# Kernel tuning notes

Measured on AMD Instinct MI355X. Metric: run time of the kernel, lower is better.

The kernel has to match this reference:

```python
import jax, jax.numpy as jnp
import numpy as np

C = 256
C8 = C // 8


def setup_inputs() -> dict:
    key = jax.random.key(0)
    ks = jax.random.split(key, 9)
    B, H, W = 4, 64, 64
    inp = jax.random.normal(ks[0], (B, C, H, W), dtype=jnp.float32)
    original = jax.random.normal(ks[1], (B, C, H, W), dtype=jnp.float32)
    s = 1.0 / np.sqrt(C)
    wq = jax.random.normal(ks[2], (C8, C), dtype=jnp.float32) * s
    bq = jax.random.normal(ks[3], (C8,), dtype=jnp.float32) * 0.01
    wk = jax.random.normal(ks[4], (C8, C), dtype=jnp.float32) * s
    bk = jax.random.normal(ks[5], (C8,), dtype=jnp.float32) * 0.01
    wv = jax.random.normal(ks[6], (C, C), dtype=jnp.float32) * s
    bv = jax.random.normal(ks[7], (C,), dtype=jnp.float32) * 0.01
    # torch inits gamma to 0; use a nonzero value so the attention branch contributes
    gamma = jnp.asarray([0.5], dtype=jnp.float32)
    return {"input": inp, "original": original, "wq": wq, "bq": bq,
            "wk": wk, "bk": bk, "wv": wv, "bv": bv, "gamma": gamma}


def reference(input, original, wq, bq, wk, bk, wv, bv, gamma):
    B, Cc, H, W = input.shape
    HW = H * W
    x = input.reshape(B, Cc, HW)          # [B, C, HW]
    o = original.reshape(B, Cc, HW)
    # 1x1 convs == per-pixel linear projections
    q = jnp.einsum('oc,bcn->bno', wq, x) + bq          # [B, HW, C8]
    k = jnp.einsum('oc,bcn->bon', wk, x) + bk[:, None]  # [B, C8, HW]
    v = jnp.einsum('oc,bcn->bon', wv, o) + bv[:, None]  # [B, C, HW]
    attn = jax.nn.softmax(jnp.einsum('bic,bcj->bij', q, k), axis=-1)  # [B, HW, HW]
    out = jnp.einsum('bcj,bij->bci', v, attn)           # [B, C, HW]
    out = out.reshape(B, Cc, H, W)
    return gamma[0] * out + input
```

## Files before the change

kernel.cpp:

```cpp
#include <hip/hip_runtime.h>

typedef short s16x8 __attribute__((ext_vector_type(8)));
typedef float f32x4 __attribute__((ext_vector_type(4)));
typedef float f32x16 __attribute__((ext_vector_type(16)));

#define B_ 4
#define C_ 256
#define S_ 4096
#define LOG2E 1.44269504088896f
#define M2 32.0f

#if __has_builtin(__builtin_amdgcn_exp2f)
#define EXP2(x) __builtin_amdgcn_exp2f(x)
#else
#define EXP2(x) __exp2f(x)
#endif

__device__ __forceinline__ unsigned short f2b(float f) {
  union { float f; unsigned u; } v; v.f = f;
  unsigned r = v.u + 0x7fffu + ((v.u >> 16) & 1u);
  return (unsigned short)(r >> 16);
}
__device__ __forceinline__ unsigned short f2b_fast(float f) {
  union { float f; unsigned u; } v; v.f = f;
  return (unsigned short)((v.u + 0x8000u) >> 16);
}
__device__ __forceinline__ s16x8 lds_ld8(const unsigned short* p) {
  union { s16x8 v; uint2 u[2]; } r;
  r.u[0] = *(const uint2*)p;
  r.u[1] = *(const uint2*)(p + 4);
  return r.v;
}

__global__ __launch_bounds__(256)
void proj_kernel(const float* __restrict__ x, const float* __restrict__ orig,
                 const float* __restrict__ wq, const float* __restrict__ bq,
                 const float* __restrict__ wk, const float* __restrict__ bk,
                 const float* __restrict__ wv, const float* __restrict__ bv,
                 unsigned short* __restrict__ Qb, unsigned short* __restrict__ Kb,
                 unsigned short* __restrict__ Vf) {
  __shared__ unsigned short Al[64 * 68];
  __shared__ unsigned short Sl[64 * 68];
  const int ct = blockIdx.x >> 6;
  const int jt = blockIdx.x & 63;
  const int n0 = jt * 64;
  const int b  = blockIdx.y;
  const int t  = threadIdx.x;
  const int L = t & 63, w = t >> 6;
  const int mt = w >> 1, nt = w & 1;
  const int g = L >> 5, l32 = L & 31;
  const float* srcb = ((ct == 0) ? x : orig) + (size_t)b * C_ * S_;
  f32x16 acc = (f32x16)0.0f;

  for (int kc = 0; kc < 4; ++kc) {
    const int k0 = kc * 64;
    __syncthreads();
    #pragma unroll
    for (int rep = 0; rep < 4; ++rep) {
      const int idx = rep * 256 + t;
      const int row = idx >> 4, c4 = (idx & 15) * 4;
      const float* wsrc; int wrow;
      if (ct == 0) {
        if (row < 32) { wsrc = wq; wrow = row; } else { wsrc = wk; wrow = row - 32; }
      } else { wsrc = wv; wrow = (ct - 1) * 64 + row; }
      f32x4 v = *(const f32x4*)(wsrc + (size_t)wrow * 256 + k0 + c4);
      union { unsigned short us[4]; uint2 u2; } pk;
      #pragma unroll
      for (int i = 0; i < 4; ++i) pk.us[i] = f2b(v[i]);
      *(uint2*)&Al[row * 68 + c4] = pk.u2;
    }
    {
      const int c4 = (t >> 4) * 4;
      const int n4 = (t & 15) * 4;
      f32x4 v0 = *(const f32x4*)(srcb + (size_t)(k0 + c4 + 0) * S_ + n0 + n4);
      f32x4 v1 = *(const f32x4*)(srcb + (size_t)(k0 + c4 + 1) * S_ + n0 + n4);
      f32x4 v2 = *(const f32x4*)(srcb + (size_t)(k0 + c4 + 2) * S_ + n0 + n4);
      f32x4 v3 = *(const f32x4*)(srcb + (size_t)(k0 + c4 + 3) * S_ + n0 + n4);
      #pragma unroll
      for (int k = 0; k < 4; ++k) {
        union { unsigned short us[4]; uint2 u2; } pk;
        pk.us[0] = f2b(v0[k]); pk.us[1] = f2b(v1[k]);
        pk.us[2] = f2b(v2[k]); pk.us[3] = f2b(v3[k]);
        *(uint2*)&Sl[(n4 + k) * 68 + c4] = pk.u2;
      }
    }
    __syncthreads();
    #pragma unroll
    for (int ks = 0; ks < 4; ++ks) {
      s16x8 af = lds_ld8(&Al[(mt * 32 + l32) * 68 + ks * 16 + g * 8]);
      s16x8 bf = lds_ld8(&Sl[(nt * 32 + l32) * 68 + ks * 16 + g * 8]);
      acc = __builtin_amdgcn_mfma_f32_32x32x16_bf16(af, bf, acc, 0, 0, 0);
    }
  }
  __syncthreads();
  unsigned short* Rl = Al;
  const int n = nt * 32 + l32;
  if (ct == 0) {
    #pragma unroll
    for (int reg = 0; reg < 16; ++reg) {
      const int rr = (reg & 3) + 8 * (reg >> 2) + 4 * g;
      const float val = (mt == 0) ? (acc[reg] + bq[rr]) * LOG2E : acc[reg] + bk[rr];
      Rl[n * 68 + mt * 32 + rr] = f2b(val);
    }
    __syncthreads();
    const int nn = t >> 2, ch0 = (t & 3) * 16;
    s16x8 a = lds_ld8(Rl + nn * 68 + ch0);
    s16x8 c = lds_ld8(Rl + nn * 68 + ch0 + 8);
    unsigned short* dst = (ch0 < 32)
        ? Qb + ((size_t)b * S_ + n0 + nn) * 32 + ch0
        : Kb + ((size_t)b * S_ + n0 + nn) * 32 + (ch0 - 32);
    *(s16x8*)dst = a;
    *(s16x8*)(dst + 8) = c;
  } else {
    const int cg = ct - 1;
    #pragma unroll
    for (int reg = 0; reg < 16; ++reg) {
      const int rr = (reg & 3) + 8 * (reg >> 2) + 4 * g;
      const int ch = mt * 32 + rr;
      Rl[ch * 68 + n] = f2b(acc[reg] + bv[cg * 64 + ch]);
    }
    __syncthreads();
    unsigned short* grp = Vf + ((size_t)(b * 64 + jt) * 4 + cg) * 4096;
    #pragma unroll
    for (int k = 0; k < 2; ++k) {
      const int G = t * 2 + k;
      const int vv = G >> 8, kb = (G >> 6) & 3, Lf = G & 63;
      const int ch64 = vv * 32 + (Lf & 31);
      const int j64  = kb * 16 + (Lf >> 5) * 8;
      s16x8 v = lds_ld8(Rl + ch64 * 68 + j64);
      *(s16x8*)(grp + G * 8) = v;
    }
  }
}

union FlashU {
  unsigned short P[64 * 68];
  float scr[2][32 * 258];
};

__global__ __launch_bounds__(512, 4)
void flash_kernel(const unsigned short* __restrict__ Qb,
                  const unsigned short* __restrict__ Kb,
                  const unsigned short* __restrict__ Vf,
                  const float* __restrict__ inp,
                  const float* __restrict__ gamma,
                  float* __restrict__ out) {
  __shared__ FlashU sm;
  __shared__ float lpart[2][64];
  __shared__ float invl[64];
  const int l  = blockIdx.x;
  const int b  = (l & 7) >> 1;
  const int i0 = ((l >> 3) * 2 + (l & 1)) * 64;
  const int t  = threadIdx.x;
  const int L = t & 63, w = t >> 6;
  const int q4 = L >> 4, c16 = L & 15;
  const int g  = L >> 5, l32 = L & 31;
  const int rh = w & 3, jh = w >> 2;
  const int cg = w & 3, dup = w >> 2;
  const float gam = gamma[0];
  const unsigned short* Kbase = Kb + (size_t)b * S_ * 32;
  const s16x8 qf = *(const s16x8*)(Qb + ((size_t)b * S_ + i0 + rh * 16 + c16) * 32 + q4 * 8);

  f32x16 acc00 = (f32x16)0.0f, acc01 = (f32x16)0.0f;
  f32x16 acc10 = (f32x16)0.0f, acc11 = (f32x16)0.0f;
  float lp[4] = {0.f, 0.f, 0.f, 0.f};

  s16x8 kc0 = *(const s16x8*)(Kbase + (size_t)(jh * 32 + c16) * 32 + q4 * 8);
  s16x8 kc1 = *(const s16x8*)(Kbase + (size_t)(jh * 32 + 16 + c16) * 32 + q4 * 8);

  for (int j0 = 0; j0 < S_; j0 += 64) {
    const int jt = j0 >> 6;
    const int jn = (j0 + 64 < S_) ? j0 + 64 : j0;
    s16x8 kn0 = *(const s16x8*)(Kbase + (size_t)(jn + jh * 32 + c16) * 32 + q4 * 8);
    s16x8 kn1 = *(const s16x8*)(Kbase + (size_t)(jn + jh * 32 + 16 + c16) * 32 + q4 * 8);
    const unsigned short* vbase = Vf + ((size_t)(b * 64 + jt) * 4 + cg) * 4096;
    s16x8 vf00 = *(const s16x8*)(vbase + (dup * 2 + 0) * 512 + L * 8);
    s16x8 vf01 = *(const s16x8*)(vbase + 2048 + (dup * 2 + 0) * 512 + L * 8);
    s16x8 vf10 = *(const s16x8*)(vbase + (dup * 2 + 1) * 512 + L * 8);
    s16x8 vf11 = *(const s16x8*)(vbase + 2048 + (dup * 2 + 1) * 512 + L * 8);
    f32x4 cinit = (f32x4)(-M2);
    f32x4 s0 = __builtin_amdgcn_mfma_f32_16x16x32_bf16(qf, kc0, cinit, 0, 0, 0);
    f32x4 s1 = __builtin_amdgcn_mfma_f32_16x16x32_bf16(qf, kc1, cinit, 0, 0, 0);
    #pragma unroll
    for (int r = 0; r < 4; ++r) {
      const float p0 = EXP2(s0[r]);
      const float p1 = EXP2(s1[r]);
      lp[r] += p0 + p1;
      const int row = rh * 16 + q4 * 4 + r;
      sm.P[row * 68 + jh * 32 + c16]      = f2b_fast(p0);
      sm.P[row * 68 + jh * 32 + 16 + c16] = f2b_fast(p1);
    }
    __syncthreads();
    {
      const int ko0 = (dup * 2 + 0) * 16 + g * 8;
      const s16x8 pf0 = lds_ld8(sm.P + l32 * 68 + ko0);
      const s16x8 pf1 = lds_ld8(sm.P + (32 + l32) * 68 + ko0);
      acc00 = __builtin_amdgcn_mfma_f32_32x32x16_bf16(pf0, vf00, acc00, 0, 0, 0);
      acc01 = __builtin_amdgcn_mfma_f32_32x32x16_bf16(pf0, vf01, acc01, 0, 0, 0);
      acc10 = __builtin_amdgcn_mfma_f32_32x32x16_bf16(pf1, vf00, acc10, 0, 0, 0);
      acc11 = __builtin_amdgcn_mfma_f32_32x32x16_bf16(pf1, vf01, acc11, 0, 0, 0);
    }
    {
      const int ko1 = (dup * 2 + 1) * 16 + g * 8;
      const s16x8 pf0 = lds_ld8(sm.P + l32 * 68 + ko1);
      const s16x8 pf1 = lds_ld8(sm.P + (32 + l32) * 68 + ko1);
      acc00 = __builtin_amdgcn_mfma_f32_32x32x16_bf16(pf0, vf10, acc00, 0, 0, 0);
      acc01 = __builtin_amdgcn_mfma_f32_32x32x16_bf16(pf0, vf11, acc01, 0, 0, 0);
      acc10 = __builtin_amdgcn_mfma_f32_32x32x16_bf16(pf1, vf10, acc10, 0, 0, 0);
      acc11 = __builtin_amdgcn_mfma_f32_32x32x16_bf16(pf1, vf11, acc11, 0, 0, 0);
    }
    __syncthreads();
    kc0 = kn0; kc1 = kn1;
  }
  #pragma unroll
  for (int r = 0; r < 4; ++r) {
    float v = lp[r];
    #pragma unroll
    for (int d = 1; d < 16; d <<= 1) v += __shfl_xor(v, d, 64);
    lp[r] = v;
  }
  if (c16 == 0) {
    #pragma unroll
    for (int r = 0; r < 4; ++r) lpart[jh][rh * 16 + q4 * 4 + r] = lp[r];
  }
  __syncthreads();
  if (t < 64) invl[t] = gam / (lpart[0][t] + lpart[1][t]);
  #pragma unroll
  for (int h = 0; h < 2; ++h) {
    const f32x16 a0 = h ? acc10 : acc00;
    const f32x16 a1 = h ? acc11 : acc01;
    float* pl = sm.scr[dup];
    #pragma unroll
    for (int reg = 0; reg < 16; ++reg) {
      const int rr = (reg & 3) + 8 * (reg >> 2) + 4 * g;
      pl[rr * 258 + cg * 64 + l32]      = a0[reg];
      pl[rr * 258 + cg * 64 + 32 + l32] = a1[reg];
    }
    __syncthreads();
    const int ch = t >> 1;
    const int il16 = (t & 1) * 16;
    #pragma unroll
    for (int q = 0; q < 4; ++q) {
      const int iloc = il16 + q * 4;
      const size_t gi = ((size_t)b * C_ + ch) * S_ + i0 + h * 32 + iloc;
      const f32x4 iv = *(const f32x4*)(inp + gi);
      f32x4 o;
      #pragma unroll
      for (int k = 0; k < 4; ++k) {
        const int il = iloc + k;
        o[k] = (sm.scr[0][il * 258 + ch] + sm.scr[1][il * 258 + ch]) * invl[h * 32 + il] + iv[k];
      }
      *(f32x4*)(out + gi) = o;
    }
    __syncthreads();
  }
}

extern "C" void kernel_launch(void* const* d_in, const int* in_sizes, int n_in,
                              void* d_out, int out_size, void* d_ws, size_t ws_size,
                              hipStream_t stream) {
  const float* inp   = (const float*)d_in[0];
  const float* orig  = (const float*)d_in[1];
  const float* wq    = (const float*)d_in[2];
  const float* bq    = (const float*)d_in[3];
  const float* wk    = (const float*)d_in[4];
  const float* bk    = (const float*)d_in[5];
  const float* wv    = (const float*)d_in[6];
  const float* bv    = (const float*)d_in[7];
  const float* gamma = (const float*)d_in[8];
  float* out = (float*)d_out;

  unsigned short* Qb = (unsigned short*)d_ws;
  unsigned short* Kb = Qb + (size_t)B_ * S_ * 32;
  unsigned short* Vf = Kb + (size_t)B_ * S_ * 32;

  proj_kernel<<<dim3(320, 4), 256, 0, stream>>>(inp, orig, wq, bq, wk, bk, wv, bv, Qb, Kb, Vf);
  flash_kernel<<<256, 512, 0, stream>>>(Qb, Kb, Vf, inp, gamma, out);
}
```

Measured before the change: 165.9 us.

## Double-buffer P tile in LDS and software-pipeline flash loop

The P tile in shared memory becomes two buffers, and the flash loop is unrolled by two. The next tile's QK^T and exp phase now overlaps with the current tile's PV MFMAs, which cuts the barriers per tile from two to one. K and V fragments are prefetched one tile ahead into register sets for even and odd tiles. This raises register pressure and LDS use, which could reduce occupancy under the 512x4 launch bounds.

Result: slower. 196.9 us (+18.7%).

```diff
diff --git a/kernel.cpp b/kernel.cpp
--- a/kernel.cpp
+++ b/kernel.cpp
@@ -134,9 +134,56 @@
 }
 
 union FlashU {
-  unsigned short P[64 * 68];
+  unsigned short P[2][64 * 68];
   float scr[2][32 * 258];
 };
+
+#define PHASE_A(PBUF, K0, K1)                                                   \
+  {                                                                             \
+    f32x4 cinit = (f32x4)(-M2);                                                 \
+    f32x4 s0 = __builtin_amdgcn_mfma_f32_16x16x32_bf16(qf, K0, cinit, 0, 0, 0); \
+    f32x4 s1 = __builtin_amdgcn_mfma_f32_16x16x32_bf16(qf, K1, cinit, 0, 0, 0); \
+    _Pragma("unroll")                                                           \
+    for (int r = 0; r < 4; ++r) {                                               \
+      const float p0 = EXP2(s0[r]);                                             \
+      const float p1 = EXP2(s1[r]);                                             \
+      lp[r] += p0 + p1;                                                         \
+      const int row = rh * 16 + q4 * 4 + r;                                     \
+      sm.P[PBUF][row * 68 + jh * 32 + c16]      = f2b_fast(p0);                 \
+      sm.P[PBUF][row * 68 + jh * 32 + 16 + c16] = f2b_fast(p1);                 \
+    }                                                                           \
+  }
+
+#define PHASE_B(PBUF, V00, V01, V10, V11)                                       \
+  {                                                                             \
+    const int ko0 = (dup * 2 + 0) * 16 + g * 8;                                 \
+    s16x8 pf0 = lds_ld8(sm.P[PBUF] + l32 * 68 + ko0);                           \
+    s16x8 pf1 = lds_ld8(sm.P[PBUF] + (32 + l32) * 68 + ko0);                    \
+    acc00 = __builtin_amdgcn_mfma_f32_32x32x16_bf16(pf0, V00, acc00, 0, 0, 0);  \
+    acc01 = __builtin_amdgcn_mfma_f32_32x32x16_bf16(pf0, V01, acc01, 0, 0, 0);  \
+    acc10 = __builtin_amdgcn_mfma_f32_32x32x16_bf16(pf1, V00, acc10, 0, 0, 0);  \
+    acc11 = __builtin_amdgcn_mfma_f32_32x32x16_bf16(pf1, V01, acc11, 0, 0, 0);  \
+    const int ko1 = (dup * 2 + 1) * 16 + g * 8;                                 \
+    pf0 = lds_ld8(sm.P[PBUF] + l32 * 68 + ko1);                                 \
+    pf1 = lds_ld8(sm.P[PBUF] + (32 + l32) * 68 + ko1);                          \
+    acc00 = __builtin_amdgcn_mfma_f32_32x32x16_bf16(pf0, V10, acc00, 0, 0, 0);  \
+    acc01 = __builtin_amdgcn_mfma_f32_32x32x16_bf16(pf0, V11, acc01, 0, 0, 0);  \
+    acc10 = __builtin_amdgcn_mfma_f32_32x32x16_bf16(pf1, V10, acc10, 0, 0, 0);  \
+    acc11 = __builtin_amdgcn_mfma_f32_32x32x16_bf16(pf1, V11, acc11, 0, 0, 0);  \
+  }
+
+#define LOAD_K(JT, K0, K1)                                                            \
+  K0 = *(const s16x8*)(Kbase + (size_t)((JT) * 64 + jh * 32 + c16) * 32 + q4 * 8);    \
+  K1 = *(const s16x8*)(Kbase + (size_t)((JT) * 64 + jh * 32 + 16 + c16) * 32 + q4 * 8);
+
+#define LOAD_V(JT, V00, V01, V10, V11)                                          \
+  {                                                                             \
+    const unsigned short* vb = Vf + ((size_t)(b * 64 + (JT)) * 4 + cg) * 4096;  \
+    V00 = *(const s16x8*)(vb + (dup * 2 + 0) * 512 + L * 8);                    \
+    V01 = *(const s16x8*)(vb + 2048 + (dup * 2 + 0) * 512 + L * 8);             \
+    V10 = *(const s16x8*)(vb + (dup * 2 + 1) * 512 + L * 8);                    \
+    V11 = *(const s16x8*)(vb + 2048 + (dup * 2 + 1) * 512 + L * 8);             \
+  }
 
 __global__ __launch_bounds__(512, 4)
 void flash_kernel(const unsigned short* __restrict__ Qb,
@@ -165,52 +212,25 @@
   f32x16 acc10 = (f32x16)0.0f, acc11 = (f32x16)0.0f;
   float lp[4] = {0.f, 0.f, 0.f, 0.f};
 
-  s16x8 kc0 = *(const s16x8*)(Kbase + (size_t)(jh * 32 + c16) * 32 + q4 * 8);
-  s16x8 kc1 = *(const s16x8*)(Kbase + (size_t)(jh * 32 + 16 + c16) * 32 + q4 * 8);
-
-  for (int j0 = 0; j0 < S_; j0 += 64) {
-    const int jt = j0 >> 6;
-    const int jn = (j0 + 64 < S_) ? j0 + 64 : j0;
-    s16x8 kn0 = *(const s16x8*)(Kbase + (size_t)(jn + jh * 32 + c16) * 32 + q4 * 8);
-    s16x8 kn1 = *(const s16x8*)(Kbase + (size_t)(jn + jh * 32 + 16 + c16) * 32 + q4 * 8);
-    const unsigned short* vbase = Vf + ((size_t)(b * 64 + jt) * 4 + cg) * 4096;
-    s16x8 vf00 = *(const s16x8*)(vbase + (dup * 2 + 0) * 512 + L * 8);
-    s16x8 vf01 = *(const s16x8*)(vbase + 2048 + (dup * 2 + 0) * 512 + L * 8);
-    s16x8 vf10 = *(const s16x8*)(vbase + (dup * 2 + 1) * 512 + L * 8);
-    s16x8 vf11 = *(const s16x8*)(vbase + 2048 + (dup * 2 + 1) * 512 + L * 8);
-    f32x4 cinit = (f32x4)(-M2);
-    f32x4 s0 = __builtin_amdgcn_mfma_f32_16x16x32_bf16(qf, kc0, cinit, 0, 0, 0);
-    f32x4 s1 = __builtin_amdgcn_mfma_f32_16x16x32_bf16(qf, kc1, cinit, 0, 0, 0);
-    #pragma unroll
-    for (int r = 0; r < 4; ++r) {
-      const float p0 = EXP2(s0[r]);
-      const float p1 = EXP2(s1[r]);
-      lp[r] += p0 + p1;
-      const int row = rh * 16 + q4 * 4 + r;
-      sm.P[row * 68 + jh * 32 + c16]      = f2b_fast(p0);
-      sm.P[row * 68 + jh * 32 + 16 + c16] = f2b_fast(p1);
-    }
+  s16x8 kE0, kE1, kO0, kO1;
+  s16x8 vE00, vE01, vE10, vE11, vO00, vO01, vO10, vO11;
+  LOAD_K(0, kE0, kE1);
+  LOAD_V(0, vE00, vE01, vE10, vE11);
+
+  for (int jt = 0; jt < 64; jt += 2) {
+    PHASE_A(0, kE0, kE1);
+    __syncthreads();
+    LOAD_K(jt + 1, kO0, kO1);
+    LOAD_V(jt + 1, vO00, vO01, vO10, vO11);
+    PHASE_B(0, vE00, vE01, vE10, vE11);
+    PHASE_A(1, kO0, kO1);
     __syncthreads();
     {
-      const int ko0 = (dup * 2 + 0) * 16 + g * 8;
-      const s16x8 pf0 = lds_ld8(sm.P + l32 * 68 + ko0);
-      const s16x8 pf1 = lds_ld8(sm.P + (32 + l32) * 68 + ko0);
-      acc00 = __builtin_amdgcn_mfma_f32_32x32x16_bf16(pf0, vf00, acc00, 0, 0, 0);
-      acc01 = __builtin_amdgcn_mfma_f32_32x32x16_bf16(pf0, vf01, acc01, 0, 0, 0);
-      acc10 = __builtin_amdgcn_mfma_f32_32x32x16_bf16(pf1, vf00, acc10, 0, 0, 0);
-      acc11 = __builtin_amdgcn_mfma_f32_32x32x16_bf16(pf1, vf01, acc11, 0, 0, 0);
-    }
-    {
-      const int ko1 = (dup * 2 + 1) * 16 + g * 8;
-      const s16x8 pf0 = lds_ld8(sm.P + l32 * 68 + ko1);
-      const s16x8 pf1 = lds_ld8(sm.P + (32 + l32) * 68 + ko1);
-      acc00 = __builtin_amdgcn_mfma_f32_32x32x16_bf16(pf0, vf10, acc00, 0, 0, 0);
-      acc01 = __builtin_amdgcn_mfma_f32_32x32x16_bf16(pf0, vf11, acc01, 0, 0, 0);
-      acc10 = __builtin_amdgcn_mfma_f32_32x32x16_bf16(pf1, vf10, acc10, 0, 0, 0);
-      acc11 = __builtin_amdgcn_mfma_f32_32x32x16_bf16(pf1, vf11, acc11, 0, 0, 0);
-    }
-    __syncthreads();
-    kc0 = kn0; kc1 = kn1;
+      const int jn = (jt + 2 < 64) ? jt + 2 : 63;
+      LOAD_K(jn, kE0, kE1);
+      LOAD_V(jn, vE00, vE01, vE10, vE11);
+    }
+    PHASE_B(1, vO00, vO01, vO10, vO11);
   }
   #pragma unroll
   for (int r = 0; r < 4; ++r) {
```

## Split output channels across two blocks and drop the split-K accumulator reduction

Applied to the files above, without the earlier changes.

The flash kernel now launches twice as many blocks, each covering half of the 256 output channels for a 64-row query tile. Each wave owns a single 32x32 accumulator over the full 64-key chunk, so the old split-K across two wave halves and its shared-memory sum in the epilogue go away. The epilogue also shrinks to one scratch pass with one barrier. In exchange, every block recomputes QK^T scores and exp for its tile, doubling that work and the K loads. Accumulator registers per thread drop, which may raise occupancy.

Measured after the change: 168.4 us. Within noise of the previous version (+1.5%).

```diff
diff --git a/kernel.cpp b/kernel.cpp
--- a/kernel.cpp
+++ b/kernel.cpp
@@ -135,7 +135,7 @@
 
 union FlashU {
   unsigned short P[64 * 68];
-  float scr[2][32 * 258];
+  float scr[128][66];
 };
 
 __global__ __launch_bounds__(512, 4)
@@ -148,24 +148,27 @@
   __shared__ FlashU sm;
   __shared__ float lpart[2][64];
   __shared__ float invl[64];
-  const int l  = blockIdx.x;
-  const int b  = (l & 7) >> 1;
-  const int i0 = ((l >> 3) * 2 + (l & 1)) * 64;
+  const int l   = blockIdx.x;
+  const int b   = (l & 7) >> 1;
+  const int chh = (l >> 3) & 1;
+  const int i0  = ((l >> 4) * 2 + (l & 1)) * 64;
   const int t  = threadIdx.x;
   const int L = t & 63, w = t >> 6;
   const int q4 = L >> 4, c16 = L & 15;
   const int g  = L >> 5, l32 = L & 31;
   const int rh = w & 3, jh = w >> 2;
-  const int cg = w & 3, dup = w >> 2;
+  const int cq = w & 3, ih = w >> 2;
   const float gam = gamma[0];
   const unsigned short* Kbase = Kb + (size_t)b * S_ * 32;
   const s16x8 qf = *(const s16x8*)(Qb + ((size_t)b * S_ + i0 + rh * 16 + c16) * 32 + q4 * 8);
 
-  f32x16 acc00 = (f32x16)0.0f, acc01 = (f32x16)0.0f;
-  f32x16 acc10 = (f32x16)0.0f, acc11 = (f32x16)0.0f;
+  const int vcg = chh * 2 + (cq >> 1);
+  const int vvv = cq & 1;
+
+  f32x16 acc = (f32x16)0.0f;
   float lp[4] = {0.f, 0.f, 0.f, 0.f};
 
-  s16x8 kc0 = *(const s16x8*)(Kbase + (size_t)(jh * 32 + c16) * 32 + q4 * 8);
+  s16x8 kc0 = *(const s16x8*)(Kbase + (size_t)(c16) * 32 + q4 * 8 + (size_t)(jh * 32) * 32);
   s16x8 kc1 = *(const s16x8*)(Kbase + (size_t)(jh * 32 + 16 + c16) * 32 + q4 * 8);
 
   for (int j0 = 0; j0 < S_; j0 += 64) {
@@ -173,11 +176,11 @@
     const int jn = (j0 + 64 < S_) ? j0 + 64 : j0;
     s16x8 kn0 = *(const s16x8*)(Kbase + (size_t)(jn + jh * 32 + c16) * 32 + q4 * 8);
     s16x8 kn1 = *(const s16x8*)(Kbase + (size_t)(jn + jh * 32 + 16 + c16) * 32 + q4 * 8);
-    const unsigned short* vbase = Vf + ((size_t)(b * 64 + jt) * 4 + cg) * 4096;
-    s16x8 vf00 = *(const s16x8*)(vbase + (dup * 2 + 0) * 512 + L * 8);
-    s16x8 vf01 = *(const s16x8*)(vbase + 2048 + (dup * 2 + 0) * 512 + L * 8);
-    s16x8 vf10 = *(const s16x8*)(vbase + (dup * 2 + 1) * 512 + L * 8);
-    s16x8 vf11 = *(const s16x8*)(vbase + 2048 + (dup * 2 + 1) * 512 + L * 8);
+    const unsigned short* vb = Vf + ((size_t)(b * 64 + jt) * 4 + vcg) * 4096 + vvv * 2048;
+    s16x8 vf0 = *(const s16x8*)(vb + 0 * 512 + L * 8);
+    s16x8 vf1 = *(const s16x8*)(vb + 1 * 512 + L * 8);
+    s16x8 vf2 = *(const s16x8*)(vb + 2 * 512 + L * 8);
+    s16x8 vf3 = *(const s16x8*)(vb + 3 * 512 + L * 8);
     f32x4 cinit = (f32x4)(-M2);
     f32x4 s0 = __builtin_amdgcn_mfma_f32_16x16x32_bf16(qf, kc0, cinit, 0, 0, 0);
     f32x4 s1 = __builtin_amdgcn_mfma_f32_16x16x32_bf16(qf, kc1, cinit, 0, 0, 0);
@@ -192,22 +195,15 @@
     }
     __syncthreads();
     {
-      const int ko0 = (dup * 2 + 0) * 16 + g * 8;
-      const s16x8 pf0 = lds_ld8(sm.P + l32 * 68 + ko0);
-      const s16x8 pf1 = lds_ld8(sm.P + (32 + l32) * 68 + ko0);
-      acc00 = __builtin_amdgcn_mfma_f32_32x32x16_bf16(pf0, vf00, acc00, 0, 0, 0);
-      acc01 = __builtin_amdgcn_mfma_f32_32x32x16_bf16(pf0, vf01, acc01, 0, 0, 0);
-      acc10 = __builtin_amdgcn_mfma_f32_32x32x16_bf16(pf1, vf00, acc10, 0, 0, 0);
-      acc11 = __builtin_amdgcn_mfma_f32_32x32x16_bf16(pf1, vf01, acc11, 0, 0, 0);
-    }
-    {
-      const int ko1 = (dup * 2 + 1) * 16 + g * 8;
-      const s16x8 pf0 = lds_ld8(sm.P + l32 * 68 + ko1);
-      const s16x8 pf1 = lds_ld8(sm.P + (32 + l32) * 68 + ko1);
-      acc00 = __builtin_amdgcn_mfma_f32_32x32x16_bf16(pf0, vf10, acc00, 0, 0, 0);
-      acc01 = __builtin_amdgcn_mfma_f32_32x32x16_bf16(pf0, vf11, acc01, 0, 0, 0);
-      acc10 = __builtin_amdgcn_mfma_f32_32x32x16_bf16(pf1, vf10, acc10, 0, 0, 0);
-      acc11 = __builtin_amdgcn_mfma_f32_32x32x16_bf16(pf1, vf11, acc11, 0, 0, 0);
+      s16x8 pf;
+      pf = lds_ld8(sm.P + (ih * 32 + l32) * 68 + 0 * 16 + g * 8);
+      acc = __builtin_amdgcn_mfma_f32_32x32x16_bf16(pf, vf0, acc, 0, 0, 0);
+      pf = lds_ld8(sm.P + (ih * 32 + l32) * 68 + 1 * 16 + g * 8);
+      acc = __builtin_amdgcn_mfma_f32_32x32x16_bf16(pf, vf1, acc, 0, 0, 0);
+      pf = lds_ld8(sm.P + (ih * 32 + l32) * 68 + 2 * 16 + g * 8);
+      acc = __builtin_amdgcn_mfma_f32_32x32x16_bf16(pf, vf2, acc, 0, 0, 0);
+      pf = lds_ld8(sm.P + (ih * 32 + l32) * 68 + 3 * 16 + g * 8);
+      acc = __builtin_amdgcn_mfma_f32_32x32x16_bf16(pf, vf3, acc, 0, 0, 0);
     }
     __syncthreads();
     kc0 = kn0; kc1 = kn1;
@@ -226,33 +222,25 @@
   __syncthreads();
   if (t < 64) invl[t] = gam / (lpart[0][t] + lpart[1][t]);
   #pragma unroll
-  for (int h = 0; h < 2; ++h) {
-    const f32x16 a0 = h ? acc10 : acc00;
-    const f32x16 a1 = h ? acc11 : acc01;
-    float* pl = sm.scr[dup];
-    #pragma unroll
-    for (int reg = 0; reg < 16; ++reg) {
-      const int rr = (reg & 3) + 8 * (reg >> 2) + 4 * g;
-      pl[rr * 258 + cg * 64 + l32]      = a0[reg];
-      pl[rr * 258 + cg * 64 + 32 + l32] = a1[reg];
-    }
-    __syncthreads();
-    const int ch = t >> 1;
-    const int il16 = (t & 1) * 16;
+  for (int reg = 0; reg < 16; ++reg) {
+    const int rr = (reg & 3) + 8 * (reg >> 2) + 4 * g;
+    sm.scr[cq * 32 + l32][ih * 32 + rr] = acc[reg];
+  }
+  __syncthreads();
+  {
+    const int ch = t >> 2;
+    const int ic = (t & 3) * 16;
     #pragma unroll
     for (int q = 0; q < 4; ++q) {
-      const int iloc = il16 + q * 4;
-      const size_t gi = ((size_t)b * C_ + ch) * S_ + i0 + h * 32 + iloc;
+      const int il = ic + q * 4;
+      const size_t gi = ((size_t)b * C_ + chh * 128 + ch) * S_ + i0 + il;
       const f32x4 iv = *(const f32x4*)(inp + gi);
       f32x4 o;
       #pragma unroll
-      for (int k = 0; k < 4; ++k) {
-        const int il = iloc + k;
-        o[k] = (sm.scr[0][il * 258 + ch] + sm.scr[1][il * 258 + ch]) * invl[h * 32 + il] + iv[k];
-      }
+      for (int k = 0; k < 4; ++k)
+        o[k] = sm.scr[ch][il + k] * invl[il + k] + iv[k];
       *(f32x4*)(out + gi) = o;
     }
-    __syncthreads();
   }
 }
 
@@ -275,5 +263,5 @@
   unsigned short* Vf = Kb + (size_t)B_ * S_ * 32;
 
   proj_kernel<<<dim3(320, 4), 256, 0, stream>>>(inp, orig, wq, bq, wk, bk, wv, bv, Qb, Kb, Vf);
-  flash_kernel<<<256, 512, 0, stream>>>(Qb, Kb, Vf, inp, gamma, out);
-}
+  flash_kernel<<<512, 512, 0, stream>>>(Qb, Kb, Vf, inp, gamma, out);
+}
```

## Pre-convert weights to bf16 and reuse staged orig tile across all V channel groups

Applied to the files above, without the earlier changes.

A new prep kernel converts the Q/K/V weights to bf16 once, with LOG2E folded into the Q weights and biases, so the projection kernel reads bf16 weights straight from global/L2 instead of converting them per block. The projection kernel now stages the whole 64-pixel x 256-channel activation tile in LDS once, and each V block loops over all four 64-channel output groups. This cuts the redundant reads of the original tensor from four to one. The cost is an extra kernel launch, fewer blocks (128x4 instead of 320x4), a larger LDS footprint, and a serial loop over channel groups inside each V block.

Result: slower. 177.9 us (+7.2%).

```diff
diff --git a/kernel.cpp b/kernel.cpp
--- a/kernel.cpp
+++ b/kernel.cpp
@@ -33,15 +33,34 @@
 }
 
 __global__ __launch_bounds__(256)
+void prep_kernel(const float* __restrict__ wq, const float* __restrict__ bq,
+                 const float* __restrict__ wk, const float* __restrict__ bk,
+                 const float* __restrict__ wv,
+                 unsigned short* __restrict__ Wb, float* __restrict__ bqk) {
+  const int t = threadIdx.x;
+  const int r = blockIdx.x * 4 + (t >> 6);
+  const int c4 = (t & 63) * 4;
+  const float* src; float scale = 1.0f;
+  if (r < 32)      { src = wq + (size_t)r * 256;        scale = LOG2E; }
+  else if (r < 64) { src = wk + (size_t)(r - 32) * 256; }
+  else             { src = wv + (size_t)(r - 64) * 256; }
+  f32x4 v = *(const f32x4*)(src + c4);
+  union { unsigned short us[4]; uint2 u2; } pk;
+  #pragma unroll
+  for (int i = 0; i < 4; ++i) pk.us[i] = f2b(v[i] * scale);
+  *(uint2*)&Wb[(size_t)r * 256 + c4] = pk.u2;
+  if (blockIdx.x == 0 && t < 64) bqk[t] = (t < 32) ? bq[t] * LOG2E : bk[t - 32];
+}
+
+__global__ __launch_bounds__(256)
 void proj_kernel(const float* __restrict__ x, const float* __restrict__ orig,
-                 const float* __restrict__ wq, const float* __restrict__ bq,
-                 const float* __restrict__ wk, const float* __restrict__ bk,
-                 const float* __restrict__ wv, const float* __restrict__ bv,
+                 const unsigned short* __restrict__ Wb,
+                 const float* __restrict__ bqk, const float* __restrict__ bv,
                  unsigned short* __restrict__ Qb, unsigned short* __restrict__ Kb,
                  unsigned short* __restrict__ Vf) {
-  __shared__ unsigned short Al[64 * 68];
-  __shared__ unsigned short Sl[64 * 68];
-  const int ct = blockIdx.x >> 6;
+  __shared__ unsigned short Sl[64 * 260];
+  __shared__ unsigned short Rl[64 * 68];
+  const int ctype = blockIdx.x >> 6;
   const int jt = blockIdx.x & 63;
   const int n0 = jt * 64;
   const int b  = blockIdx.y;
@@ -49,29 +68,14 @@
   const int L = t & 63, w = t >> 6;
   const int mt = w >> 1, nt = w & 1;
   const int g = L >> 5, l32 = L & 31;
-  const float* srcb = ((ct == 0) ? x : orig) + (size_t)b * C_ * S_;
-  f32x16 acc = (f32x16)0.0f;
-
-  for (int kc = 0; kc < 4; ++kc) {
-    const int k0 = kc * 64;
-    __syncthreads();
-    #pragma unroll
-    for (int rep = 0; rep < 4; ++rep) {
-      const int idx = rep * 256 + t;
-      const int row = idx >> 4, c4 = (idx & 15) * 4;
-      const float* wsrc; int wrow;
-      if (ct == 0) {
-        if (row < 32) { wsrc = wq; wrow = row; } else { wsrc = wk; wrow = row - 32; }
-      } else { wsrc = wv; wrow = (ct - 1) * 64 + row; }
-      f32x4 v = *(const f32x4*)(wsrc + (size_t)wrow * 256 + k0 + c4);
-      union { unsigned short us[4]; uint2 u2; } pk;
-      #pragma unroll
-      for (int i = 0; i < 4; ++i) pk.us[i] = f2b(v[i]);
-      *(uint2*)&Al[row * 68 + c4] = pk.u2;
-    }
-    {
-      const int c4 = (t >> 4) * 4;
-      const int n4 = (t & 15) * 4;
+  const float* srcb = ((ctype == 0) ? x : orig) + (size_t)b * C_ * S_;
+
+  {
+    const int c4 = (t >> 4) * 4;
+    const int n4 = (t & 15) * 4;
+    #pragma unroll
+    for (int kc = 0; kc < 4; ++kc) {
+      const int k0 = kc * 64;
       f32x4 v0 = *(const f32x4*)(srcb + (size_t)(k0 + c4 + 0) * S_ + n0 + n4);
       f32x4 v1 = *(const f32x4*)(srcb + (size_t)(k0 + c4 + 1) * S_ + n0 + n4);
       f32x4 v2 = *(const f32x4*)(srcb + (size_t)(k0 + c4 + 2) * S_ + n0 + n4);
@@ -81,26 +85,28 @@
         union { unsigned short us[4]; uint2 u2; } pk;
         pk.us[0] = f2b(v0[k]); pk.us[1] = f2b(v1[k]);
         pk.us[2] = f2b(v2[k]); pk.us[3] = f2b(v3[k]);
-        *(uint2*)&Sl[(n4 + k) * 68 + c4] = pk.u2;
-      }
-    }
-    __syncthreads();
-    #pragma unroll
-    for (int ks = 0; ks < 4; ++ks) {
-      s16x8 af = lds_ld8(&Al[(mt * 32 + l32) * 68 + ks * 16 + g * 8]);
-      s16x8 bf = lds_ld8(&Sl[(nt * 32 + l32) * 68 + ks * 16 + g * 8]);
-      acc = __builtin_amdgcn_mfma_f32_32x32x16_bf16(af, bf, acc, 0, 0, 0);
+        *(uint2*)&Sl[(n4 + k) * 260 + k0 + c4] = pk.u2;
+      }
     }
   }
   __syncthreads();
-  unsigned short* Rl = Al;
+
   const int n = nt * 32 + l32;
-  if (ct == 0) {
+  if (ctype == 0) {
+    f32x16 acc = (f32x16)0.0f;
+    #pragma unroll
+    for (int kc = 0; kc < 4; ++kc) {
+      #pragma unroll
+      for (int ks = 0; ks < 4; ++ks) {
+        const s16x8 af = *(const s16x8*)(Wb + (size_t)(mt * 32 + l32) * 256 + kc * 64 + ks * 16 + g * 8);
+        const s16x8 bf = lds_ld8(&Sl[(nt * 32 + l32) * 260 + kc * 64 + ks * 16 + g * 8]);
+        acc = __builtin_amdgcn_mfma_f32_32x32x16_bf16(af, bf, acc, 0, 0, 0);
+      }
+    }
     #pragma unroll
     for (int reg = 0; reg < 16; ++reg) {
       const int rr = (reg & 3) + 8 * (reg >> 2) + 4 * g;
-      const float val = (mt == 0) ? (acc[reg] + bq[rr]) * LOG2E : acc[reg] + bk[rr];
-      Rl[n * 68 + mt * 32 + rr] = f2b(val);
+      Rl[n * 68 + mt * 32 + rr] = f2b(acc[reg] + bqk[mt * 32 + rr]);
     }
     __syncthreads();
     const int nn = t >> 2, ch0 = (t & 3) * 16;
@@ -112,23 +118,37 @@
     *(s16x8*)dst = a;
     *(s16x8*)(dst + 8) = c;
   } else {
-    const int cg = ct - 1;
-    #pragma unroll
-    for (int reg = 0; reg < 16; ++reg) {
-      const int rr = (reg & 3) + 8 * (reg >> 2) + 4 * g;
-      const int ch = mt * 32 + rr;
-      Rl[ch * 68 + n] = f2b(acc[reg] + bv[cg * 64 + ch]);
-    }
-    __syncthreads();
-    unsigned short* grp = Vf + ((size_t)(b * 64 + jt) * 4 + cg) * 4096;
-    #pragma unroll
-    for (int k = 0; k < 2; ++k) {
-      const int G = t * 2 + k;
-      const int vv = G >> 8, kb = (G >> 6) & 3, Lf = G & 63;
-      const int ch64 = vv * 32 + (Lf & 31);
-      const int j64  = kb * 16 + (Lf >> 5) * 8;
-      s16x8 v = lds_ld8(Rl + ch64 * 68 + j64);
-      *(s16x8*)(grp + G * 8) = v;
+    #pragma unroll 1
+    for (int cg = 0; cg < 4; ++cg) {
+      f32x16 acc = (f32x16)0.0f;
+      const unsigned short* Wg = Wb + (size_t)(64 + cg * 64 + mt * 32 + l32) * 256;
+      #pragma unroll
+      for (int kc = 0; kc < 4; ++kc) {
+        #pragma unroll
+        for (int ks = 0; ks < 4; ++ks) {
+          const s16x8 af = *(const s16x8*)(Wg + kc * 64 + ks * 16 + g * 8);
+          const s16x8 bf = lds_ld8(&Sl[(nt * 32 + l32) * 260 + kc * 64 + ks * 16 + g * 8]);
+          acc = __builtin_amdgcn_mfma_f32_32x32x16_bf16(af, bf, acc, 0, 0, 0);
+        }
+      }
+      #pragma unroll
+      for (int reg = 0; reg < 16; ++reg) {
+        const int rr = (reg & 3) + 8 * (reg >> 2) + 4 * g;
+        const int ch = mt * 32 + rr;
+        Rl[ch * 68 + n] = f2b(acc[reg] + bv[cg * 64 + ch]);
+      }
+      __syncthreads();
+      unsigned short* grp = Vf + ((size_t)(b * 64 + jt) * 4 + cg) * 4096;
+      #pragma unroll
+      for (int k = 0; k < 2; ++k) {
+        const int G = t * 2 + k;
+        const int vv = G >> 8, kb = (G >> 6) & 3, Lf = G & 63;
+        const int ch64 = vv * 32 + (Lf & 31);
+        const int j64  = kb * 16 + (Lf >> 5) * 8;
+        s16x8 v = lds_ld8(Rl + ch64 * 68 + j64);
+        *(s16x8*)(grp + G * 8) = v;
+      }
+      __syncthreads();
     }
   }
 }
@@ -273,7 +293,10 @@
   unsigned short* Qb = (unsigned short*)d_ws;
   unsigned short* Kb = Qb + (size_t)B_ * S_ * 32;
   unsigned short* Vf = Kb + (size_t)B_ * S_ * 32;
-
-  proj_kernel<<<dim3(320, 4), 256, 0, stream>>>(inp, orig, wq, bq, wk, bk, wv, bv, Qb, Kb, Vf);
+  unsigned short* Wb = Vf + (size_t)B_ * 64 * 4 * 4096;
+  float* bqk = (float*)(Wb + 320 * 256);
+
+  prep_kernel<<<80, 256, 0, stream>>>(wq, bq, wk, bk, wv, Wb, bqk);
+  proj_kernel<<<dim3(128, 4), 256, 0, stream>>>(inp, orig, Wb, bqk, bv, Qb, Kb, Vf);
   flash_kernel<<<256, 512, 0, stream>>>(Qb, Kb, Vf, inp, gamma, out);
 }
```
